# Kernel tuning notes

Hardware: AMD Instinct MI355X
Metric: run time of the kernel (lower is better)

Reference implementation:

```python
import jax, jax.numpy as jnp
import numpy as np

B, S, H = 2, 2048, 1024
NH, HD = 16, 64
WIN = 256
EPS = 1e-5


def _layernorm(x, g, b):
    # normalize over last dim (head_dim)
    m = jnp.mean(x, axis=-1, keepdims=True)
    v = jnp.mean((x - m) ** 2, axis=-1, keepdims=True)
    return (x - m) * jax.lax.rsqrt(v + EPS) * g + b


def setup_inputs() -> dict:
    key = jax.random.key(0)
    ks = jax.random.split(key, 6)
    scale = 1.0 / np.sqrt(2.0 * H)  # ~ xavier_uniform with gain 1/sqrt(2)
    inp = {
        "x": jax.random.normal(ks[0], (B, S, H), dtype=jnp.float32),
        "Wq": jax.random.normal(ks[1], (H, H), dtype=jnp.float32) * scale,
        "bq": jnp.zeros((H,), jnp.float32),
        "Wk": jax.random.normal(ks[2], (H, H), dtype=jnp.float32) * scale,
        "bk": jnp.zeros((H,), jnp.float32),
        "Wv": jax.random.normal(ks[3], (H, H), dtype=jnp.float32) * scale,
        "bv": jnp.zeros((H,), jnp.float32),
        "Wo": jax.random.normal(ks[4], (H, H), dtype=jnp.float32) * scale,
        "bo": jnp.zeros((H,), jnp.float32),
        "ln_q_w": jnp.ones((HD,), jnp.float32),
        "ln_q_b": jnp.zeros((HD,), jnp.float32),
        "ln_k_w": jnp.ones((HD,), jnp.float32),
        "ln_k_b": jnp.zeros((HD,), jnp.float32),
    }
    return inp


def reference(x, Wq, bq, Wk, bk, Wv, bv, Wo, bo, ln_q_w, ln_q_b, ln_k_w, ln_k_b):
    b, s, _ = x.shape
    # projections (torch Linear: x @ W.T + b)
    q = (x @ Wq.T + bq).reshape(b, s, NH, HD)
    k = (x @ Wk.T + bk).reshape(b, s, NH, HD)
    v = (x @ Wv.T + bv).reshape(b, s, NH, HD)
    # QK layernorm over head_dim
    q = _layernorm(q, ln_q_w, ln_q_b)
    k = _layernorm(k, ln_k_w, ln_k_b)
    # scores [b, h, s, s]
    scores = jnp.einsum("bqhd,bkhd->bhqk", q, k) / np.sqrt(HD).astype(np.float32)
    i = jnp.arange(s)[:, None]
    j = jnp.arange(s)[None, :]
    mask = (j <= i) & (i - j <= WIN)
    scores = jnp.where(mask[None, None], scores, -jnp.inf)
    probs = jax.nn.softmax(scores, axis=-1)
    out = jnp.einsum("bhqk,bkhd->bqhd", probs, v).reshape(b, s, NH * HD)
    return out @ Wo.T + bo
```

## Files before the change

### kernel.cpp

```cpp
#include <hip/hip_runtime.h>
#include <hip/hip_bf16.h>
#include <cstdint>

typedef __hip_bfloat16 bf16;
typedef __attribute__((ext_vector_type(8))) short s16x8;
typedef __attribute__((ext_vector_type(4))) float f32x4;

#define NB_B 2
#define NB_S 2048
#define NB_H 1024
#define NB_NH 16
#define NB_HD 64
#define NB_WIN 256
#define NTOK 4096

static __device__ __forceinline__ unsigned pack_bf16(float a, float b) {
    bf16 ta = __float2bfloat16(a), tb = __float2bfloat16(b);
    return (unsigned)*(unsigned short*)&ta | ((unsigned)*(unsigned short*)&tb << 16);
}
static __device__ __forceinline__ unsigned short bf16u(float a) {
    bf16 t = __float2bfloat16(a);
    return *(unsigned short*)&t;
}

#define VMCNT(n) asm volatile("s_waitcnt vmcnt(" #n ")" ::: "memory")
#define SBAR __builtin_amdgcn_s_barrier()
#define LGKM0 do { asm volatile("s_waitcnt lgkmcnt(0)" ::: "memory"); \
                   __builtin_amdgcn_sched_barrier(0); } while (0)

__global__ void k_castall(const float* __restrict__ x, const float* __restrict__ Wq,
                          const float* __restrict__ Wk, const float* __restrict__ Wv,
                          const float* __restrict__ Wo,
                          bf16* __restrict__ xb, bf16* __restrict__ wqkvb,
                          bf16* __restrict__ wob) {
    int idx = blockIdx.x * blockDim.x + threadIdx.x;
    const float* in; bf16* out; int i;
    if (idx < 1048576)        { in = x;  out = xb;              i = idx * 4; }
    else if (idx < 1310720)   { in = Wq; out = wqkvb;           i = (idx - 1048576) * 4; }
    else if (idx < 1572864)   { in = Wk; out = wqkvb + 1048576; i = (idx - 1310720) * 4; }
    else if (idx < 1835008)   { in = Wv; out = wqkvb + 2097152; i = (idx - 1572864) * 4; }
    else                      { in = Wo; out = wob;             i = (idx - 1835008) * 4; }
    const float4 v = *(const float4*)(in + i);
    ushort4 u;
    u.x = bf16u(v.x); u.y = bf16u(v.y); u.z = bf16u(v.z); u.w = bf16u(v.w);
    *(ushort4*)((unsigned short*)out + i) = u;
}

#define G2_STAGE(AD, BD, KT)                                                         \
    do {                                                                             \
        _Pragma("unroll")                                                            \
        for (int it_ = 0; it_ < 4; ++it_) {                                          \
            int c_ = it_ * 512 + tid;                                                \
            int row_ = c_ >> 3, pc_ = c_ & 7;                                        \
            int col_ = ((pc_ ^ (row_ & 7)) << 3);                                    \
            __builtin_amdgcn_global_load_lds(                                        \
                (const __attribute__((address_space(1))) void*)(Ap + (size_t)(m0 + row_) * 1024 + (KT) + col_), \
                (__attribute__((address_space(3))) void*)((AD) + c_ * 8), 16, 0, 0); \
            __builtin_amdgcn_global_load_lds(                                        \
                (const __attribute__((address_space(1))) void*)(Bp + (size_t)(n0 + row_) * 1024 + (KT) + col_), \
                (__attribute__((address_space(3))) void*)((BD) + c_ * 8), 16, 0, 0); \
        }                                                                            \
        __builtin_amdgcn_sched_barrier(0);                                           \
    } while (0)

#define G2_READS_A(AS, P)                                                            \
    _Pragma("unroll")                                                                \
    for (int j_ = 0; j_ < 2; ++j_)                                                   \
        _Pragma("unroll")                                                            \
        for (int kk_ = 0; kk_ < 2; ++kk_)                                            \
            af_[j_][kk_] = *(const s16x8*)&(AS)[(wr * 128 + ((P) * 2 + j_) * 16 + q) * 64 \
                                                + ((((kk_ << 2) + g) ^ (q & 7)) << 3)];

#define G2_MFMA(P)                                                                   \
    __builtin_amdgcn_s_setprio(1);                                                   \
    _Pragma("unroll")                                                                \
    for (int kk_ = 0; kk_ < 2; ++kk_)                                                \
        _Pragma("unroll")                                                            \
        for (int j_ = 0; j_ < 2; ++j_)                                               \
            _Pragma("unroll")                                                        \
            for (int ni_ = 0; ni_ < 4; ++ni_)                                        \
                acc[(P) * 2 + j_][ni_] = __builtin_amdgcn_mfma_f32_16x16x32_bf16(    \
                    af_[j_][kk_], bf_[ni_][kk_], acc[(P) * 2 + j_][ni_], 0, 0, 0);   \
    __builtin_amdgcn_s_setprio(0);

#define G2_TILE(AS, BS, AN, BN_, KTN)                                                \
    do {                                                                             \
        s16x8 af_[2][2], bf_[4][2];                                                  \
        G2_READS_A(AS, 0);                                                           \
        _Pragma("unroll")                                                            \
        for (int ni_ = 0; ni_ < 4; ++ni_)                                            \
            _Pragma("unroll")                                                        \
            for (int kk_ = 0; kk_ < 2; ++kk_)                                        \
                bf_[ni_][kk_] = *(const s16x8*)&(BS)[(wc * 64 + ni_ * 16 + q) * 64   \
                                                     + ((((kk_ << 2) + g) ^ (q & 7)) << 3)]; \
        if ((KTN) < 1024) { G2_STAGE(AN, BN_, KTN); }                                \
        SBAR; LGKM0;                                                                 \
        G2_MFMA(0);                                                                  \
        SBAR;                                                                        \
        G2_READS_A(AS, 1); SBAR; LGKM0; G2_MFMA(1); SBAR;                            \
        G2_READS_A(AS, 2); SBAR; LGKM0; G2_MFMA(2); SBAR;                            \
        G2_READS_A(AS, 3); SBAR; LGKM0; G2_MFMA(3);                                  \
        VMCNT(0); SBAR;                                                              \
    } while (0)

__global__ __launch_bounds__(512, 2) void k_gemm_qkv(const bf16* __restrict__ Ap,
                                                  const bf16* __restrict__ Bp,
                                                  const float* __restrict__ bq,
                                                  const float* __restrict__ bk,
                                                  const float* __restrict__ bv,
                                                  const float* __restrict__ lqw,
                                                  const float* __restrict__ lqb,
                                                  const float* __restrict__ lkw,
                                                  const float* __restrict__ lkb,
                                                  bf16* __restrict__ qbuf,
                                                  bf16* __restrict__ kbuf,
                                                  bf16* __restrict__ vtb) {
    __shared__ bf16 As0[256 * 64], As1[256 * 64];
    __shared__ bf16 Bs0[256 * 64], Bs1[256 * 64];
    const int tid = threadIdx.x;
    const int lane = tid & 63;
    const int wid = tid >> 6;
    const int wr = wid >> 2, wc = wid & 3;

    const int orig = blockIdx.y * gridDim.x + blockIdx.x;
    const int wk = (orig & 7) * 24 + (orig >> 3);
    const int m0 = (wk / 12) * 256, n0 = (wk % 12) * 256;

    const int g = lane >> 4, q = lane & 15;

    f32x4 acc[8][4] = {};

    G2_STAGE(As0, Bs0, 0);
    VMCNT(0); SBAR;

#pragma unroll 1
    for (int t = 0; t < 16; t += 2) {
        G2_TILE(As0, Bs0, As1, Bs1, t * 64 + 64);
        G2_TILE(As1, Bs1, As0, Bs0, t * 64 + 128);
    }

    const int col0 = n0 + wc * 64;
    const int hh = col0 >> 6;
    const int csub = col0 & 1023;
    const float* bias = (hh < 16) ? bq : (hh < 32) ? bk : bv;

    float bcol[4];
#pragma unroll
    for (int ni = 0; ni < 4; ++ni) bcol[ni] = bias[csub + ni * 16 + q];
#pragma unroll
    for (int mi = 0; mi < 8; ++mi)
#pragma unroll
        for (int ni = 0; ni < 4; ++ni)
#pragma unroll
            for (int r = 0; r < 4; ++r) acc[mi][ni][r] += bcol[ni];

    if (hh < 32) {
        const float* gwa = (hh < 16) ? lqw : lkw;
        const float* gba = (hh < 16) ? lqb : lkb;
        float gam[4], bet[4];
#pragma unroll
        for (int ni = 0; ni < 4; ++ni) {
            gam[ni] = gwa[ni * 16 + q];
            bet[ni] = gba[ni * 16 + q];
        }
        bf16* outp = (hh < 16) ? qbuf : kbuf;
#pragma unroll
        for (int mi = 0; mi < 8; ++mi)
#pragma unroll
            for (int r = 0; r < 4; ++r) {
                float s1 = acc[mi][0][r] + acc[mi][1][r] + acc[mi][2][r] + acc[mi][3][r];
                float s2 = acc[mi][0][r] * acc[mi][0][r] + acc[mi][1][r] * acc[mi][1][r]
                         + acc[mi][2][r] * acc[mi][2][r] + acc[mi][3][r] * acc[mi][3][r];
#pragma unroll
                for (int mm = 1; mm < 16; mm <<= 1) {
                    s1 += __shfl_xor(s1, mm, 64);
                    s2 += __shfl_xor(s2, mm, 64);
                }
                float mean = s1 * (1.f / 64.f);
                float var = s2 * (1.f / 64.f) - mean * mean;
                float rs = rsqrtf(var + 1e-5f);
                int token = m0 + wr * 128 + mi * 16 + g * 4 + r;
#pragma unroll
                for (int ni = 0; ni < 4; ++ni) {
                    float y = (acc[mi][ni][r] - mean) * rs * gam[ni] + bet[ni];
                    outp[(size_t)token * 1024 + csub + ni * 16 + q] = __float2bfloat16(y);
                }
            }
    } else {
        const int b = m0 >> 11;
        const int bh = b * 16 + (csub >> 6);
        const int sbase0 = (m0 & 2047) + wr * 128 + g * 4;
#pragma unroll
        for (int mi = 0; mi < 8; ++mi) {
            const int sb = sbase0 + mi * 16;
#pragma unroll
            for (int ni = 0; ni < 4; ++ni) {
                const int d = ni * 16 + q;
                ushort4 u;
                u.x = bf16u(acc[mi][ni][0]); u.y = bf16u(acc[mi][ni][1]);
                u.z = bf16u(acc[mi][ni][2]); u.w = bf16u(acc[mi][ni][3]);
                *(ushort4*)(vtb + ((size_t)bh * 64 + d) * 2048 + sb) = u;
            }
        }
    }
}

#define G_STAGE(AD, BD, KT)                                                          \
    do {                                                                             \
        _Pragma("unroll")                                                            \
        for (int it_ = 0; it_ < 4; ++it_) {                                          \
            int c_ = it_ * 256 + tid;                                                \
            int row_ = c_ >> 3, pc_ = c_ & 7;                                        \
            int col_ = ((pc_ ^ (row_ & 7)) << 3);                                    \
            __builtin_amdgcn_global_load_lds(                                        \
                (const __attribute__((address_space(1))) void*)(Ap + (size_t)(m0 + row_) * 1024 + (KT) + col_), \
                (__attribute__((address_space(3))) void*)((AD) + c_ * 8), 16, 0, 0); \
            __builtin_amdgcn_global_load_lds(                                        \
                (const __attribute__((address_space(1))) void*)(Bp + (size_t)(n0 + row_) * 1024 + (KT) + col_), \
                (__attribute__((address_space(3))) void*)((BD) + c_ * 8), 16, 0, 0); \
        }                                                                            \
        __builtin_amdgcn_sched_barrier(0);                                           \
    } while (0)

#define G_COMPUTE(AS, BS)                                                            \
    do {                                                                             \
        _Pragma("unroll")                                                            \
        for (int kk_ = 0; kk_ < 2; ++kk_) {                                          \
            const int rchunk_ = (((kk_ << 2) + g) ^ (q & 7)) << 3;                   \
            s16x8 af_[4], bf_[4];                                                    \
            _Pragma("unroll")                                                        \
            for (int mi_ = 0; mi_ < 4; ++mi_)                                        \
                af_[mi_] = *(const s16x8*)&(AS)[(wr * 64 + mi_ * 16 + q) * 64 + rchunk_]; \
            _Pragma("unroll")                                                        \
            for (int ni_ = 0; ni_ < 4; ++ni_)                                        \
                bf_[ni_] = *(const s16x8*)&(BS)[(wc * 64 + ni_ * 16 + q) * 64 + rchunk_]; \
            __builtin_amdgcn_s_setprio(1);                                           \
            _Pragma("unroll")                                                        \
            for (int mi_ = 0; mi_ < 4; ++mi_)                                        \
                _Pragma("unroll")                                                    \
                for (int ni_ = 0; ni_ < 4; ++ni_)                                    \
                    acc[mi_][ni_] = __builtin_amdgcn_mfma_f32_16x16x32_bf16(         \
                        af_[mi_], bf_[ni_], acc[mi_][ni_], 0, 0, 0);                 \
            __builtin_amdgcn_s_setprio(0);                                           \
        }                                                                            \
    } while (0)

#define G_MAINLOOP                                                                   \
    G_STAGE(As0, Bs0, 0);                                                            \
    G_STAGE(As1, Bs1, 64);                                                           \
    for (int i_ = 0; i_ < 7; ++i_) {                                                 \
        const int kt_ = i_ * 128;                                                    \
        VMCNT(8); SBAR;                                                              \
        G_COMPUTE(As0, Bs0);                                                         \
        SBAR;                                                                        \
        G_STAGE(As0, Bs0, kt_ + 128);                                                \
        VMCNT(8); SBAR;                                                              \
        G_COMPUTE(As1, Bs1);                                                         \
        SBAR;                                                                        \
        G_STAGE(As1, Bs1, kt_ + 192);                                                \
    }                                                                                \
    VMCNT(8); SBAR;                                                                  \
    G_COMPUTE(As0, Bs0);                                                             \
    VMCNT(0); SBAR;                                                                  \
    G_COMPUTE(As1, Bs1)

__global__ __launch_bounds__(256) void k_gemm_out(const bf16* __restrict__ Ap,
                                                  const bf16* __restrict__ Bp,
                                                  const float* __restrict__ bias,
                                                  float* __restrict__ Cv) {
    __shared__ bf16 As0[128 * 64], As1[128 * 64];
    __shared__ bf16 Bs0[128 * 64], Bs1[128 * 64];
    const int tid = threadIdx.x;
    const int lane = tid & 63;
    const int w = tid >> 6;
    const int wr = w >> 1, wc = w & 1;

    const int orig = blockIdx.y * gridDim.x + blockIdx.x;
    const int wk = (orig & 7) * 32 + (orig >> 3);
    const int m0 = (wk / 8) * 128, n0 = (wk % 8) * 128;

    const int g = lane >> 4, q = lane & 15;

    f32x4 acc[4][4] = {};

    G_MAINLOOP;

#pragma unroll
    for (int mi = 0; mi < 4; ++mi)
#pragma unroll
        for (int ni = 0; ni < 4; ++ni) {
            int colg = n0 + wc * 64 + ni * 16 + q;
            float bcol = bias[colg];
#pragma unroll
            for (int r = 0; r < 4; ++r) {
                int rowg = m0 + wr * 64 + mi * 16 + g * 4 + r;
                Cv[(size_t)rowg * 1024 + colg] = acc[mi][ni][r] + bcol;
            }
        }
}

#undef G_STAGE
#undef G_COMPUTE
#undef G_MAINLOOP

__global__ __launch_bounds__(256) void k_attn(const bf16* __restrict__ qb,
                                              const bf16* __restrict__ kb,
                                              const bf16* __restrict__ vt,
                                              bf16* __restrict__ att) {
    __shared__ bf16 Ks[2][32 * 64];
    __shared__ bf16 Vs[2][64 * 32];

    const int orig = blockIdx.y * gridDim.x + blockIdx.x;
    const int wk = (orig & 7) * 128 + (orig >> 3);
    const int q0 = (wk & 31) * 64;
    const int bh = wk >> 5;

    const int b = bh >> 4, h = bh & 15;
    const int tid = threadIdx.x;
    const int w = tid >> 6;
    const int lane = tid & 63;
    const int g = lane >> 4, qi = lane & 15;
    const int qw0 = q0 + w * 16;
    const int iq = qw0 + qi;

    const size_t qbase = ((size_t)(b * 2048 + iq)) * 1024 + h * 64 + g * 8;
    s16x8 bq0 = *(const s16x8*)(qb + qbase);
    s16x8 bq1 = *(const s16x8*)(qb + qbase + 32);

    f32x4 o[4] = {};
    float lp = 0.f;

    int jmin = q0 - NB_WIN; if (jmin < 0) jmin = 0;
    const int c0 = jmin >> 5;
    const int c1 = (q0 + 63) >> 5;

    const int krow = tid >> 3, kpc = tid & 7;
    const int kcol = ((kpc ^ (krow & 7)) << 3);
    const int vrow = tid >> 2, vpc = tid & 3;
    const int vcol = ((vpc ^ (vrow & 3)) << 3);
    const bf16* kbase = kb + ((size_t)(b * 2048 + krow)) * 1024 + h * 64 + kcol;
    const bf16* vbase = vt + ((size_t)bh * 64 + vrow) * 2048 + vcol;

    __builtin_amdgcn_global_load_lds(
        (const __attribute__((address_space(1))) void*)(kbase + (size_t)(c0 * 32) * 1024),
        (__attribute__((address_space(3))) void*)(&Ks[0][tid * 8]), 16, 0, 0);
    __builtin_amdgcn_global_load_lds(
        (const __attribute__((address_space(1))) void*)(vbase + c0 * 32),
        (__attribute__((address_space(3))) void*)(&Vs[0][tid * 8]), 16, 0, 0);

    int buf = 0;
    for (int c = c0; c <= c1; ++c) {
        const int ks = c * 32;
        if (c < c1) {
            const int ksn = ks + 32;
            __builtin_amdgcn_global_load_lds(
                (const __attribute__((address_space(1))) void*)(kbase + (size_t)ksn * 1024),
                (__attribute__((address_space(3))) void*)(&Ks[buf ^ 1][tid * 8]), 16, 0, 0);
            __builtin_amdgcn_global_load_lds(
                (const __attribute__((address_space(1))) void*)(vbase + ksn),
                (__attribute__((address_space(3))) void*)(&Vs[buf ^ 1][tid * 8]), 16, 0, 0);
            __builtin_amdgcn_sched_barrier(0);
            VMCNT(2);
        } else {
            VMCNT(0);
        }
        SBAR;

        if (ks + 31 >= qw0 - NB_WIN && ks <= qw0 + 15) {
            const int ch0 = ((g ^ (qi & 7)) << 3);
            const bf16* kr0 = &Ks[buf][qi * 64];
            const bf16* kr1 = &Ks[buf][(16 + qi) * 64];
            s16x8 a00 = *(const s16x8*)(kr0 + ch0);
            s16x8 a01 = *(const s16x8*)(kr0 + (ch0 ^ 32));
            s16x8 a10 = *(const s16x8*)(kr1 + ch0);
            s16x8 a11 = *(const s16x8*)(kr1 + (ch0 ^ 32));

            f32x4 s0 = {}, s1 = {};
            s0 = __builtin_amdgcn_mfma_f32_16x16x32_bf16(a00, bq0, s0, 0, 0, 0);
            s0 = __builtin_amdgcn_mfma_f32_16x16x32_bf16(a01, bq1, s0, 0, 0, 0);
            s1 = __builtin_amdgcn_mfma_f32_16x16x32_bf16(a10, bq0, s1, 0, 0, 0);
            s1 = __builtin_amdgcn_mfma_f32_16x16x32_bf16(a11, bq1, s1, 0, 0, 0);

            float p0[4], p1[4];
#pragma unroll
            for (int r = 0; r < 4; ++r) {
                int j0 = ks + 4 * g + r, j1 = j0 + 16;
                p0[r] = ((unsigned)(iq - j0) <= (unsigned)NB_WIN)
                            ? __expf(s0[r] * 0.125f - 8.f) : 0.f;
                p1[r] = ((unsigned)(iq - j1) <= (unsigned)NB_WIN)
                            ? __expf(s1[r] * 0.125f - 8.f) : 0.f;
                lp += p0[r] + p1[r];
            }
            unsigned P0 = pack_bf16(p0[0], p0[1]), P1 = pack_bf16(p0[2], p0[3]);
            unsigned Q0 = pack_bf16(p1[0], p1[1]), Q1 = pack_bf16(p1[2], p1[3]);

            const int srcA = qi + (g & 1) * 32;
            const int srcB = srcA + 16;
            unsigned tP0a = __shfl((int)P0, srcA, 64), tQ0a = __shfl((int)Q0, srcA, 64);
            unsigned tP1a = __shfl((int)P1, srcA, 64), tQ1a = __shfl((int)Q1, srcA, 64);
            unsigned tP0b = __shfl((int)P0, srcB, 64), tQ0b = __shfl((int)Q0, srcB, 64);
            unsigned tP1b = __shfl((int)P1, srcB, 64), tQ1b = __shfl((int)Q1, srcB, 64);
            union { s16x8 v; unsigned u[4]; } pa;
            pa.u[0] = (g < 2) ? tP0a : tQ0a;
            pa.u[1] = (g < 2) ? tP1a : tQ1a;
            pa.u[2] = (g < 2) ? tP0b : tQ0b;
            pa.u[3] = (g < 2) ? tP1b : tQ1b;

            const int chv = ((g ^ (qi & 3)) << 3);
#pragma unroll
            for (int db = 0; db < 4; ++db) {
                s16x8 bv = *(const s16x8*)&Vs[buf][(db * 16 + qi) * 32 + chv];
                o[db] = __builtin_amdgcn_mfma_f32_16x16x32_bf16(pa.v, bv, o[db], 0, 0, 0);
            }
        }

        SBAR;
        buf ^= 1;
    }

    float l2 = lp + __shfl_xor(lp, 16, 64);
    float lf = l2 + __shfl_xor(l2, 32, 64);
    float lr[4];
#pragma unroll
    for (int r = 0; r < 4; ++r) lr[r] = __shfl(lf, 4 * g + r, 64);

#pragma unroll
    for (int db = 0; db < 4; ++db)
#pragma unroll
        for (int r = 0; r < 4; ++r) {
            float vlu = o[db][r] / lr[r];
            att[((size_t)(b * 2048 + qw0 + 4 * g + r)) * 1024 + h * 64 + db * 16 + qi] =
                __float2bfloat16(vlu);
        }
}

extern "C" void kernel_launch(void* const* d_in, const int* in_sizes, int n_in,
                              void* d_out, int out_size, void* d_ws, size_t ws_size,
                              hipStream_t stream) {
    const float* x   = (const float*)d_in[0];
    const float* Wq  = (const float*)d_in[1];
    const float* bq  = (const float*)d_in[2];
    const float* Wk  = (const float*)d_in[3];
    const float* bk  = (const float*)d_in[4];
    const float* Wv  = (const float*)d_in[5];
    const float* bv  = (const float*)d_in[6];
    const float* Wo  = (const float*)d_in[7];
    const float* bo  = (const float*)d_in[8];
    const float* lqw = (const float*)d_in[9];
    const float* lqb = (const float*)d_in[10];
    const float* lkw = (const float*)d_in[11];
    const float* lkb = (const float*)d_in[12];

    char* ws = (char*)d_ws;
    bf16* xb    = (bf16*)(ws + 0);
    bf16* wqkvb = (bf16*)(ws + 8388608);
    bf16* wob   = (bf16*)(ws + 14680064);
    bf16* qbuf  = (bf16*)(ws + 16777216);
    bf16* kbuf  = (bf16*)(ws + 25165824);
    bf16* vtb   = (bf16*)(ws + 33554432);
    bf16* attb  = (bf16*)(ws + 41943040);

    k_castall<<<8192, 256, 0, stream>>>(x, Wq, Wk, Wv, Wo, xb, wqkvb, wob);

    k_gemm_qkv<<<dim3(12, 16), 512, 0, stream>>>(xb, wqkvb, bq, bk, bv,
                                                 lqw, lqb, lkw, lkb,
                                                 qbuf, kbuf, vtb);

    k_attn<<<dim3(32, 32), 256, 0, stream>>>(qbuf, kbuf, vtb, attb);

    k_gemm_out<<<dim3(8, 32), 256, 0, stream>>>(attb, wob, bo, (float*)d_out);
}
```

Measured before the change: 95.04 us.

## Restructure QKV GEMM global-to-LDS staging into finer-grained interleaved prefetch pipeline

```diff
diff --git a/kernel.cpp b/kernel.cpp
--- a/kernel.cpp
+++ b/kernel.cpp
@@ -46,24 +46,16 @@
     *(ushort4*)((unsigned short*)out + i) = u;
 }
 
-#define G2_STAGE(AD, BD, KT)                                                         \
+#define Q8_STG(DSTBASE, SRC, GROW, KT)                                               \
     do {                                                                             \
-        _Pragma("unroll")                                                            \
-        for (int it_ = 0; it_ < 4; ++it_) {                                          \
-            int c_ = it_ * 512 + tid;                                                \
-            int row_ = c_ >> 3, pc_ = c_ & 7;                                        \
-            int col_ = ((pc_ ^ (row_ & 7)) << 3);                                    \
-            __builtin_amdgcn_global_load_lds(                                        \
-                (const __attribute__((address_space(1))) void*)(Ap + (size_t)(m0 + row_) * 1024 + (KT) + col_), \
-                (__attribute__((address_space(3))) void*)((AD) + c_ * 8), 16, 0, 0); \
-            __builtin_amdgcn_global_load_lds(                                        \
-                (const __attribute__((address_space(1))) void*)(Bp + (size_t)(n0 + row_) * 1024 + (KT) + col_), \
-                (__attribute__((address_space(3))) void*)((BD) + c_ * 8), 16, 0, 0); \
-        }                                                                            \
-        __builtin_amdgcn_sched_barrier(0);                                           \
+        int row_ = tid >> 3, pc_ = tid & 7;                                          \
+        int col_ = ((pc_ ^ (row_ & 7)) << 3);                                        \
+        __builtin_amdgcn_global_load_lds(                                            \
+            (const __attribute__((address_space(1))) void*)((SRC) + (size_t)((GROW) + row_) * 1024 + (KT) + col_), \
+            (__attribute__((address_space(3))) void*)((DSTBASE) + tid * 8), 16, 0, 0); \
     } while (0)
 
-#define G2_READS_A(AS, P)                                                            \
+#define Q8_RDA(AS, P)                                                                \
     _Pragma("unroll")                                                                \
     for (int j_ = 0; j_ < 2; ++j_)                                                   \
         _Pragma("unroll")                                                            \
@@ -71,7 +63,7 @@
             af_[j_][kk_] = *(const s16x8*)&(AS)[(wr * 128 + ((P) * 2 + j_) * 16 + q) * 64 \
                                                 + ((((kk_ << 2) + g) ^ (q & 7)) << 3)];
 
-#define G2_MFMA(P)                                                                   \
+#define Q8_MM(P)                                                                     \
     __builtin_amdgcn_s_setprio(1);                                                   \
     _Pragma("unroll")                                                                \
     for (int kk_ = 0; kk_ < 2; ++kk_)                                                \
@@ -83,24 +75,45 @@
                     af_[j_][kk_], bf_[ni_][kk_], acc[(P) * 2 + j_][ni_], 0, 0, 0);   \
     __builtin_amdgcn_s_setprio(0);
 
-#define G2_TILE(AS, BS, AN, BN_, KTN)                                                \
+#define Q8_TILE(CA, CB, NA, NB_P, KT1, KT2, DO_A13, DO_T2, VM)                       \
     do {                                                                             \
         s16x8 af_[2][2], bf_[4][2];                                                  \
-        G2_READS_A(AS, 0);                                                           \
+        Q8_RDA(CA, 0);                                                               \
         _Pragma("unroll")                                                            \
         for (int ni_ = 0; ni_ < 4; ++ni_)                                            \
             _Pragma("unroll")                                                        \
             for (int kk_ = 0; kk_ < 2; ++kk_)                                        \
-                bf_[ni_][kk_] = *(const s16x8*)&(BS)[(wc * 64 + ni_ * 16 + q) * 64   \
+                bf_[ni_][kk_] = *(const s16x8*)&(CB)[(wc * 64 + ni_ * 16 + q) * 64   \
                                                      + ((((kk_ << 2) + g) ^ (q & 7)) << 3)]; \
-        if ((KTN) < 1024) { G2_STAGE(AN, BN_, KTN); }                                \
-        SBAR; LGKM0;                                                                 \
-        G2_MFMA(0);                                                                  \
+        if (DO_A13) {                                                                \
+            Q8_STG((NA) + 4096, Ap, m0 + 64, KT1);                                   \
+            Q8_STG((NA) + 12288, Ap, m0 + 192, KT1);                                 \
+        }                                                                            \
+        __builtin_amdgcn_sched_barrier(0);                                           \
+        SBAR; LGKM0; Q8_MM(0); SBAR;                                                 \
+        Q8_RDA(CA, 1);                                                               \
+        if (DO_T2) {                                                                 \
+            Q8_STG((CB) + 0, Bp, n0 + 0, KT2);                                       \
+            Q8_STG((CB) + 4096, Bp, n0 + 64, KT2);                                   \
+        }                                                                            \
+        __builtin_amdgcn_sched_barrier(0);                                           \
+        SBAR; LGKM0; Q8_MM(1); SBAR;                                                 \
+        Q8_RDA(CA, 2);                                                               \
+        if (DO_T2) {                                                                 \
+            Q8_STG((CB) + 8192, Bp, n0 + 128, KT2);                                  \
+            Q8_STG((CB) + 12288, Bp, n0 + 192, KT2);                                 \
+        }                                                                            \
+        __builtin_amdgcn_sched_barrier(0);                                           \
+        SBAR; LGKM0; Q8_MM(2); SBAR;                                                 \
+        Q8_RDA(CA, 3);                                                               \
+        if (DO_T2) {                                                                 \
+            Q8_STG((CA) + 0, Ap, m0 + 0, KT2);                                       \
+            Q8_STG((CA) + 8192, Ap, m0 + 128, KT2);                                  \
+        }                                                                            \
+        __builtin_amdgcn_sched_barrier(0);                                           \
+        SBAR; LGKM0; Q8_MM(3);                                                       \
+        VM;                                                                          \
         SBAR;                                                                        \
-        G2_READS_A(AS, 1); SBAR; LGKM0; G2_MFMA(1); SBAR;                            \
-        G2_READS_A(AS, 2); SBAR; LGKM0; G2_MFMA(2); SBAR;                            \
-        G2_READS_A(AS, 3); SBAR; LGKM0; G2_MFMA(3);                                  \
-        VMCNT(0); SBAR;                                                              \
     } while (0)
 
 __global__ __launch_bounds__(512, 2) void k_gemm_qkv(const bf16* __restrict__ Ap,
@@ -115,8 +128,11 @@
                                                   bf16* __restrict__ qbuf,
                                                   bf16* __restrict__ kbuf,
                                                   bf16* __restrict__ vtb) {
-    __shared__ bf16 As0[256 * 64], As1[256 * 64];
-    __shared__ bf16 Bs0[256 * 64], Bs1[256 * 64];
+    __shared__ bf16 As[2 * 256 * 64];
+    __shared__ bf16 Bs[2 * 256 * 64];
+    bf16* A0 = As;            bf16* A1 = As + 16384;
+    bf16* B0 = Bs;            bf16* B1 = Bs + 16384;
+
     const int tid = threadIdx.x;
     const int lane = tid & 63;
     const int wid = tid >> 6;
@@ -130,14 +146,23 @@
 
     f32x4 acc[8][4] = {};
 
-    G2_STAGE(As0, Bs0, 0);
-    VMCNT(0); SBAR;
-
-#pragma unroll 1
-    for (int t = 0; t < 16; t += 2) {
-        G2_TILE(As0, Bs0, As1, Bs1, t * 64 + 64);
-        G2_TILE(As1, Bs1, As0, Bs0, t * 64 + 128);
+    Q8_STG(A0 + 0, Ap, m0 + 0, 0);    Q8_STG(A0 + 4096, Ap, m0 + 64, 0);
+    Q8_STG(A0 + 8192, Ap, m0 + 128, 0); Q8_STG(A0 + 12288, Ap, m0 + 192, 0);
+    Q8_STG(B0 + 0, Bp, n0 + 0, 0);    Q8_STG(B0 + 4096, Bp, n0 + 64, 0);
+    Q8_STG(B0 + 8192, Bp, n0 + 128, 0); Q8_STG(B0 + 12288, Bp, n0 + 192, 0);
+    Q8_STG(B1 + 0, Bp, n0 + 0, 64);   Q8_STG(B1 + 4096, Bp, n0 + 64, 64);
+    Q8_STG(B1 + 8192, Bp, n0 + 128, 64); Q8_STG(B1 + 12288, Bp, n0 + 192, 64);
+    Q8_STG(A1 + 0, Ap, m0 + 0, 64);   Q8_STG(A1 + 8192, Ap, m0 + 128, 64);
+    __builtin_amdgcn_sched_barrier(0);
+    VMCNT(6); SBAR;
+
+    for (int tt = 0; tt < 14; tt += 2) {
+        const int k1 = tt * 64;
+        Q8_TILE(A0, B0, A1, B1, k1 + 64, k1 + 128, 1, 1, VMCNT(6));
+        Q8_TILE(A1, B1, A0, B0, k1 + 128, k1 + 192, 1, 1, VMCNT(6));
     }
+    Q8_TILE(A0, B0, A1, B1, 960, 0, 1, 0, VMCNT(0));
+    Q8_TILE(A1, B1, A0, B0, 0, 0, 0, 0, (void)0);
 
     const int col0 = n0 + wc * 64;
     const int hh = col0 >> 6;
```

Result: no change. 94.83 us (-0.2%).
